# Performance work log

Hardware: AMD Instinct MI355X
Metric: run time of the kernel (lower is better)

## Reference

```python
import jax, jax.numpy as jnp
import numpy as np

B, C, IN, H = 64, 128, 1024, 512  # batch, channels, input features (=='seq_length' arg), hidden


def setup_inputs() -> dict:
    key = jax.random.key(0)
    ks = jax.random.split(key, 9)
    s = 1.0 / np.sqrt(H)  # PyTorch LSTM init: U(-1/sqrt(H), 1/sqrt(H))
    u = lambda k, shape: jax.random.uniform(k, shape, jnp.float32, -s, s)
    return {
        "x": jax.random.normal(ks[0], (B, C, IN), jnp.float32),
        # layer 0: one weight set per direction (fwd, bwd)
        "W_ih0": u(ks[1], (2, 4 * H, IN)),
        "W_hh0": u(ks[2], (2, 4 * H, H)),
        "b_ih0": u(ks[3], (2, 4 * H)),
        "b_hh0": u(ks[4], (2, 4 * H)),
        # layers 1..2: input is concat of both directions (2H)
        "W_ih12": u(ks[5], (2, 2, 4 * H, 2 * H)),
        "W_hh12": u(ks[6], (2, 2, 4 * H, H)),
        "b_ih12": u(ks[7], (2, 2, 4 * H)),
        "b_hh12": u(ks[8], (2, 2, 4 * H)),
    }


def _cell(inp, W_ih, b_ih, b_hh):
    # One LSTM step from zero state (h0 = c0 = 0): W_hh @ h0 == 0, f*c0 == 0.
    gates = inp @ W_ih.T + b_ih + b_hh  # [N, 4H]
    i, f, g, o = jnp.split(gates, 4, axis=-1)  # PyTorch gate order: i, f, g, o
    c = jax.nn.sigmoid(i) * jnp.tanh(g)
    return jax.nn.sigmoid(o) * jnp.tanh(c)  # h, shape [N, H]


def reference(x, W_ih0, W_hh0, b_ih0, b_hh0, W_ih12, W_hh12, b_ih12, b_hh12):
    b, c, n = x.shape
    # Each channel is an independent seq-len-1 LSTM call with zero init state,
    # so fold channels into the batch dimension. W_hh* contribute nothing (h0=0).
    xb = x.reshape(b * c, n)
    h = jnp.concatenate(
        [_cell(xb, W_ih0[d], b_ih0[d], b_hh0[d]) for d in range(2)], axis=-1
    )  # [b*c, 2H]
    for l in range(2):  # layers 1 and 2
        h = jnp.concatenate(
            [_cell(h, W_ih12[l, d], b_ih12[l, d], b_hh12[l, d]) for d in range(2)],
            axis=-1,
        )
    return h.reshape(b, c, 2 * H)  # [batch, channels, 2*hidden]
```

## Files before the change

### kernel.cpp

```cpp
#include <hip/hip_runtime.h>


typedef float f32x4 __attribute__((ext_vector_type(4)));
typedef short short8 __attribute__((ext_vector_type(8)));
typedef unsigned short u16;

#define NP 3072
#define MROWS 8192
#define KDIM 1024
#define BM 256
#define BN 192
#define BK 32
#define LDS_TILE 28672

__device__ __forceinline__ u16 f2bf(float f) {
  unsigned u = __float_as_uint(f);
  u += 0x7fffu + ((u >> 16) & 1u);
  return (u16)(u >> 16);
}
__device__ __forceinline__ float sigmoid_f(float x) {
  return 1.0f / (1.0f + __expf(-x));
}
__device__ __forceinline__ float tanh_f(float x) {
  float xc = fminf(fmaxf(x, -15.0f), 15.0f);
  float e = __expf(2.0f * xc);
  return (e - 1.0f) / (e + 1.0f);
}
__device__ __forceinline__ void gload_lds16(const void* g, void* l) {
  __builtin_amdgcn_global_load_lds((const __attribute__((address_space(1))) void*)g,
                                   (__attribute__((address_space(3))) void*)l,
                                   16, 0, 0);
}


__global__ __launch_bounds__(256) void k_convert_x(const float* __restrict__ x,
                                                   u16* __restrict__ out) {
  int tid = blockIdx.x * 256 + threadIdx.x;
  const float4* src = (const float4*)x + (size_t)tid * 2;
  float4 v0 = src[0], v1 = src[1];
  union { u16 u[8]; uint4 v; } r;
  r.u[0] = f2bf(v0.x); r.u[1] = f2bf(v0.y); r.u[2] = f2bf(v0.z); r.u[3] = f2bf(v0.w);
  r.u[4] = f2bf(v1.x); r.u[5] = f2bf(v1.y); r.u[6] = f2bf(v1.z); r.u[7] = f2bf(v1.w);
  ((uint4*)out)[tid] = r.v;
}

__global__ __launch_bounds__(256) void k_pack_w(const float* __restrict__ Wih0,
                                                const float* __restrict__ Wih12,
                                                u16* __restrict__ P) {
  int tid = blockIdx.x * 256 + threadIdx.x;
  int s   = tid / (NP * 128);
  int rem = tid - s * (NP * 128);
  int p   = rem >> 7;
  int k8  = rem & 127;
  int hb = p / 48;
  int pr = p - hb * 48;
  int gs = pr >> 4;
  int hl = pr & 15;
  int hcol = hb * 16 + hl;
  int dir = hcol >> 9;
  int h   = hcol & 511;
  int og  = (gs == 0) ? 0 : (gs + 1);
  const float* src;
  if (s == 0)
    src = Wih0 + ((size_t)(dir * 2048 + og * 512 + h)) * 1024 + k8 * 8;
  else
    src = Wih12 + ((size_t)(((s - 1) * 2 + dir) * 2048 + og * 512 + h)) * 1024 + k8 * 8;
  float4 v0 = ((const float4*)src)[0];
  float4 v1 = ((const float4*)src)[1];
  union { u16 u[8]; uint4 v; } r;
  r.u[0] = f2bf(v0.x); r.u[1] = f2bf(v0.y); r.u[2] = f2bf(v0.z); r.u[3] = f2bf(v0.w);
  r.u[4] = f2bf(v1.x); r.u[5] = f2bf(v1.y); r.u[6] = f2bf(v1.z); r.u[7] = f2bf(v1.w);
  ((uint4*)P)[tid] = r.v;
}

__global__ __launch_bounds__(256) void k_pack_bias(const float* __restrict__ bih0,
                                                   const float* __restrict__ bhh0,
                                                   const float* __restrict__ bih12,
                                                   const float* __restrict__ bhh12,
                                                   float* __restrict__ pb) {
  int tid = blockIdx.x * 256 + threadIdx.x;
  if (tid >= 3 * NP) return;
  int s = tid / NP;
  int p = tid - s * NP;
  int hb = p / 48;
  int pr = p - hb * 48;
  int gs = pr >> 4;
  int hl = pr & 15;
  int hcol = hb * 16 + hl;
  int dir = hcol >> 9;
  int h   = hcol & 511;
  int og  = (gs == 0) ? 0 : (gs + 1);
  int j   = og * 512 + h;
  float v;
  if (s == 0) {
    int i = dir * 2048 + j;
    v = bih0[i] + bhh0[i];
  } else {
    int i = ((s - 1) * 2 + dir) * 2048 + j;
    v = bih12[i] + bhh12[i];
  }
  pb[tid] = v;
}


#define BAR()    __builtin_amdgcn_s_barrier()
#define SCHEDB() __builtin_amdgcn_sched_barrier(0)
#define WAITV(N) asm volatile("s_waitcnt vmcnt(" #N ")" ::: "memory")
#define MM(Macc, Aop, Bop) Macc = __builtin_amdgcn_mfma_f32_16x16x32_bf16(Aop, Bop, Macc, 0, 0, 0)

#define STAGE(BUF, KT) \
  { char* dst = lds + (BUF) * LDS_TILE + t * 16; \
    gload_lds16(srcA + (size_t)(KT) * BK,               dst); \
    gload_lds16(srcA + 64 * KDIM + (size_t)(KT) * BK,   dst + 4096); \
    gload_lds16(srcA + 128 * KDIM + (size_t)(KT) * BK,  dst + 8192); \
    gload_lds16(srcA + 192 * KDIM + (size_t)(KT) * BK,  dst + 12288); \
    gload_lds16(srcB + (size_t)(KT) * BK,               dst + 16384); \
    gload_lds16(srcB + 64 * KDIM + (size_t)(KT) * BK,   dst + 20480); \
    gload_lds16(srcB + 128 * KDIM + (size_t)(KT) * BK,  dst + 24576); }

#define KSTEP(RBUF, KT, DOST, LASTT) \
  { \
    if (DOST) { STAGE((RBUF)^1, (KT)+1); } \
    const char* base = lds + (RBUF) * LDS_TILE; \
    short8 a0 = *(const short8*)(base + aBase); \
    short8 a1 = *(const short8*)(base + aBase + 1024); \
    short8 a2 = *(const short8*)(base + aBase + 2048); \
    short8 a3 = *(const short8*)(base + aBase + 3072); \
    short8 b0 = *(const short8*)(base + bBase); \
    short8 b1 = *(const short8*)(base + bBase + 1024); \
    short8 b2 = *(const short8*)(base + bBase + 2048); \
    short8 b3 = *(const short8*)(base + bBase + 3072); \
    short8 b4 = *(const short8*)(base + bBase + 4096); \
    short8 b5 = *(const short8*)(base + bBase + 5120); \
    __builtin_amdgcn_s_setprio(1); \
    MM(acc[0][0], a0, b0); MM(acc[1][0], a1, b0); MM(acc[2][0], a2, b0); MM(acc[3][0], a3, b0); \
    MM(acc[0][1], a0, b1); MM(acc[1][1], a1, b1); MM(acc[2][1], a2, b1); MM(acc[3][1], a3, b1); \
    MM(acc[0][2], a0, b2); MM(acc[1][2], a1, b2); MM(acc[2][2], a2, b2); MM(acc[3][2], a3, b2); \
    MM(acc[0][3], a0, b3); MM(acc[1][3], a1, b3); MM(acc[2][3], a2, b3); MM(acc[3][3], a3, b3); \
    MM(acc[0][4], a0, b4); MM(acc[1][4], a1, b4); MM(acc[2][4], a2, b4); MM(acc[3][4], a3, b4); \
    MM(acc[0][5], a0, b5); MM(acc[1][5], a1, b5); MM(acc[2][5], a2, b5); MM(acc[3][5], a3, b5); \
    __builtin_amdgcn_s_setprio(0); \
    a0 = *(const short8*)(base + aBase + 4096); \
    a1 = *(const short8*)(base + aBase + 5120); \
    a2 = *(const short8*)(base + aBase + 6144); \
    a3 = *(const short8*)(base + aBase + 7168); \
    __builtin_amdgcn_s_setprio(1); \
    MM(acc[4][0], a0, b0); MM(acc[5][0], a1, b0); MM(acc[6][0], a2, b0); MM(acc[7][0], a3, b0); \
    MM(acc[4][1], a0, b1); MM(acc[5][1], a1, b1); MM(acc[6][1], a2, b1); MM(acc[7][1], a3, b1); \
    MM(acc[4][2], a0, b2); MM(acc[5][2], a1, b2); MM(acc[6][2], a2, b2); MM(acc[7][2], a3, b2); \
    MM(acc[4][3], a0, b3); MM(acc[5][3], a1, b3); MM(acc[6][3], a2, b3); MM(acc[7][3], a3, b3); \
    MM(acc[4][4], a0, b4); MM(acc[5][4], a1, b4); MM(acc[6][4], a2, b4); MM(acc[7][4], a3, b4); \
    MM(acc[4][5], a0, b5); MM(acc[5][5], a1, b5); MM(acc[6][5], a2, b5); MM(acc[7][5], a3, b5); \
    __builtin_amdgcn_s_setprio(0); \
    if (!(LASTT)) { WAITV(0); BAR(); SCHEDB(); } \
  }

template <bool F32OUT>
__global__ __launch_bounds__(256) void k_lstm_gemm2b(const u16* __restrict__ A,
                                                     const u16* __restrict__ Bp,
                                                     const float* __restrict__ bias,
                                                     void* __restrict__ outp) {
  __shared__ __align__(16) char lds[2 * LDS_TILE];
  const int t    = threadIdx.x;
  const int lane = t & 63;
  const int w    = t >> 6;
  const int wr   = w >> 1;
  const int wc   = w & 1;
  const int r16  = lane & 15, kg = lane >> 4;

  const int n_hw = blockIdx.y * gridDim.x + blockIdx.x;
  const int c    = n_hw & 7;
  const int wlc  = n_hw >> 3;
  const int bx   = (c & 1) * 8 + (wlc & 7);
  const int by   = (c >> 1) * 8 + (wlc >> 3);
  const int brow = by * BM;
  const int bn0  = bx * BN;

  const int slot = (kg ^ ((r16 >> 1) & 3)) << 4;
  const int aBase = wr * 8192 + r16 * 64 + slot;
  const int bBase = 16384 + wc * 6144 + r16 * 64 + slot;

  const int srow = t >> 2;
  const int koct = ((t & 3) ^ ((t >> 3) & 3)) << 3;
  const u16* srcA = A  + (size_t)(brow + srow) * KDIM + koct;
  const u16* srcB = Bp + (size_t)(bn0  + srow) * KDIM + koct;

  f32x4 acc[8][6];
#pragma unroll
  for (int m = 0; m < 8; ++m)
#pragma unroll
    for (int n = 0; n < 6; ++n) acc[m][n] = (f32x4){0.f, 0.f, 0.f, 0.f};

  STAGE(0, 0);
  WAITV(0);
  BAR(); SCHEDB();

  for (int k2 = 0; k2 < 15; ++k2) {
    KSTEP(0, 2 * k2, 1, 0);
    KSTEP(1, 2 * k2 + 1, 1, 0);
  }
  KSTEP(0, 30, 1, 0);
  KSTEP(1, 31, 0, 1);

#pragma unroll
  for (int trio = 0; trio < 2; ++trio) {
    int pbase = bn0 + wc * 96 + trio * 48;
    float biV = bias[pbase + r16];
    float bgV = bias[pbase + 16 + r16];
    float boV = bias[pbase + 32 + r16];
    int hcol = (bx * 4 + wc * 2 + trio) * 16 + r16;
#pragma unroll
    for (int m = 0; m < 8; ++m) {
      int rowb = brow + wr * 128 + m * 16 + kg * 4;
#pragma unroll
      for (int r = 0; r < 4; ++r) {
        float vi = acc[m][trio * 3 + 0][r] + biV;
        float vg = acc[m][trio * 3 + 1][r] + bgV;
        float vo = acc[m][trio * 3 + 2][r] + boV;
        float c2 = sigmoid_f(vi) * tanh_f(vg);
        float hv = sigmoid_f(vo) * tanh_f(c2);
        size_t oidx = (size_t)(rowb + r) * 1024 + hcol;
        if (F32OUT) ((float*)outp)[oidx] = hv;
        else        ((u16*)outp)[oidx]   = f2bf(hv);
      }
    }
  }
}

extern "C" void kernel_launch(void* const* d_in, const int* in_sizes, int n_in,
                              void* d_out, int out_size, void* d_ws, size_t ws_size,
                              hipStream_t stream) {
  const float* x     = (const float*)d_in[0];
  const float* Wih0  = (const float*)d_in[1];
  const float* bih0  = (const float*)d_in[3];
  const float* bhh0  = (const float*)d_in[4];
  const float* Wih12 = (const float*)d_in[5];
  const float* bih12 = (const float*)d_in[7];
  const float* bhh12 = (const float*)d_in[8];

  char* ws = (char*)d_ws;
  u16*   xbf = (u16*)ws;
  u16*   h1  = (u16*)(ws + 16777216);
  u16*   h2  = (u16*)(ws + 33554432);
  u16*   P3  = (u16*)(ws + 50331648);
  float* pb3 = (float*)(ws + 69206016);

  k_convert_x<<<4096, 256, 0, stream>>>(x, xbf);
  k_pack_w<<<4608, 256, 0, stream>>>(Wih0, Wih12, P3);
  k_pack_bias<<<36, 256, 0, stream>>>(bih0, bhh0, bih12, bhh12, pb3);

  dim3 grid(NP / BN, MROWS / BM);
  k_lstm_gemm2b<false><<<grid, 256, 0, stream>>>(xbf, P3, pb3, h1);
  k_lstm_gemm2b<false><<<grid, 256, 0, stream>>>(h1, P3 + (size_t)NP * KDIM, pb3 + NP, h2);
  k_lstm_gemm2b<true ><<<grid, 256, 0, stream>>>(h2, P3 + (size_t)2 * NP * KDIM, pb3 + 2 * NP, d_out);
}
```

Before: 228.4 us.

## Switch GEMM to 512-thread blocks with triple-buffered LDS pipeline

```diff
diff --git a/kernel.cpp b/kernel.cpp
--- a/kernel.cpp
+++ b/kernel.cpp
@@ -110,17 +110,14 @@
 
 #define STAGE(BUF, KT) \
   { char* dst = lds + (BUF) * LDS_TILE + t * 16; \
-    gload_lds16(srcA + (size_t)(KT) * BK,               dst); \
-    gload_lds16(srcA + 64 * KDIM + (size_t)(KT) * BK,   dst + 4096); \
-    gload_lds16(srcA + 128 * KDIM + (size_t)(KT) * BK,  dst + 8192); \
-    gload_lds16(srcA + 192 * KDIM + (size_t)(KT) * BK,  dst + 12288); \
-    gload_lds16(srcB + (size_t)(KT) * BK,               dst + 16384); \
-    gload_lds16(srcB + 64 * KDIM + (size_t)(KT) * BK,   dst + 20480); \
-    gload_lds16(srcB + 128 * KDIM + (size_t)(KT) * BK,  dst + 24576); }
-
-#define KSTEP(RBUF, KT, DOST, LASTT) \
+    gload_lds16(srcA + (size_t)(KT) * BK,              dst); \
+    gload_lds16(srcA + 128 * KDIM + (size_t)(KT) * BK, dst + 8192); \
+    gload_lds16(srcB + (size_t)(KT) * BK,              dst + 16384); \
+    if (t < 256) { gload_lds16(srcB + 128 * KDIM + (size_t)(KT) * BK, dst + 24576); } }
+
+#define KSTEP(RBUF, SBUF, KT, DOST, LASTT) \
   { \
-    if (DOST) { STAGE((RBUF)^1, (KT)+1); } \
+    if (DOST) { STAGE(SBUF, (KT) + 2); } \
     const char* base = lds + (RBUF) * LDS_TILE; \
     short8 a0 = *(const short8*)(base + aBase); \
     short8 a1 = *(const short8*)(base + aBase + 1024); \
@@ -140,27 +137,17 @@
     MM(acc[0][4], a0, b4); MM(acc[1][4], a1, b4); MM(acc[2][4], a2, b4); MM(acc[3][4], a3, b4); \
     MM(acc[0][5], a0, b5); MM(acc[1][5], a1, b5); MM(acc[2][5], a2, b5); MM(acc[3][5], a3, b5); \
     __builtin_amdgcn_s_setprio(0); \
-    a0 = *(const short8*)(base + aBase + 4096); \
-    a1 = *(const short8*)(base + aBase + 5120); \
-    a2 = *(const short8*)(base + aBase + 6144); \
-    a3 = *(const short8*)(base + aBase + 7168); \
-    __builtin_amdgcn_s_setprio(1); \
-    MM(acc[4][0], a0, b0); MM(acc[5][0], a1, b0); MM(acc[6][0], a2, b0); MM(acc[7][0], a3, b0); \
-    MM(acc[4][1], a0, b1); MM(acc[5][1], a1, b1); MM(acc[6][1], a2, b1); MM(acc[7][1], a3, b1); \
-    MM(acc[4][2], a0, b2); MM(acc[5][2], a1, b2); MM(acc[6][2], a2, b2); MM(acc[7][2], a3, b2); \
-    MM(acc[4][3], a0, b3); MM(acc[5][3], a1, b3); MM(acc[6][3], a2, b3); MM(acc[7][3], a3, b3); \
-    MM(acc[4][4], a0, b4); MM(acc[5][4], a1, b4); MM(acc[6][4], a2, b4); MM(acc[7][4], a3, b4); \
-    MM(acc[4][5], a0, b5); MM(acc[5][5], a1, b5); MM(acc[6][5], a2, b5); MM(acc[7][5], a3, b5); \
-    __builtin_amdgcn_s_setprio(0); \
-    if (!(LASTT)) { WAITV(0); BAR(); SCHEDB(); } \
+    if (DOST) { if (t < 256) { WAITV(4); } else { WAITV(3); } } \
+    else if (!(LASTT)) { WAITV(0); } \
+    if (!(LASTT)) { BAR(); SCHEDB(); } \
   }
 
 template <bool F32OUT>
-__global__ __launch_bounds__(256) void k_lstm_gemm2b(const u16* __restrict__ A,
-                                                     const u16* __restrict__ Bp,
-                                                     const float* __restrict__ bias,
-                                                     void* __restrict__ outp) {
-  __shared__ __align__(16) char lds[2 * LDS_TILE];
+__global__ __launch_bounds__(512) void k_lstm_tri(const u16* __restrict__ A,
+                                                  const u16* __restrict__ Bp,
+                                                  const float* __restrict__ bias,
+                                                  void* __restrict__ outp) {
+  __shared__ __align__(16) char lds[3 * LDS_TILE];
   const int t    = threadIdx.x;
   const int lane = t & 63;
   const int w    = t >> 6;
@@ -177,7 +164,7 @@
   const int bn0  = bx * BN;
 
   const int slot = (kg ^ ((r16 >> 1) & 3)) << 4;
-  const int aBase = wr * 8192 + r16 * 64 + slot;
+  const int aBase = wr * 4096 + r16 * 64 + slot;
   const int bBase = 16384 + wc * 6144 + r16 * 64 + slot;
 
   const int srow = t >> 2;
@@ -185,22 +172,24 @@
   const u16* srcA = A  + (size_t)(brow + srow) * KDIM + koct;
   const u16* srcB = Bp + (size_t)(bn0  + srow) * KDIM + koct;
 
-  f32x4 acc[8][6];
-#pragma unroll
-  for (int m = 0; m < 8; ++m)
+  f32x4 acc[4][6];
+#pragma unroll
+  for (int m = 0; m < 4; ++m)
 #pragma unroll
     for (int n = 0; n < 6; ++n) acc[m][n] = (f32x4){0.f, 0.f, 0.f, 0.f};
 
   STAGE(0, 0);
-  WAITV(0);
+  STAGE(1, 1);
+  if (t < 256) { WAITV(4); } else { WAITV(3); }
   BAR(); SCHEDB();
 
-  for (int k2 = 0; k2 < 15; ++k2) {
-    KSTEP(0, 2 * k2, 1, 0);
-    KSTEP(1, 2 * k2 + 1, 1, 0);
-  }
-  KSTEP(0, 30, 1, 0);
-  KSTEP(1, 31, 0, 1);
+  for (int k3 = 0; k3 < 10; ++k3) {
+    KSTEP(0, 2, k3 * 3 + 0, 1, 0);
+    KSTEP(1, 0, k3 * 3 + 1, 1, 0);
+    KSTEP(2, 1, k3 * 3 + 2, 1, 0);
+  }
+  KSTEP(0, 0, 30, 0, 0);
+  KSTEP(1, 0, 31, 0, 1);
 
 #pragma unroll
   for (int trio = 0; trio < 2; ++trio) {
@@ -210,8 +199,8 @@
     float boV = bias[pbase + 32 + r16];
     int hcol = (bx * 4 + wc * 2 + trio) * 16 + r16;
 #pragma unroll
-    for (int m = 0; m < 8; ++m) {
-      int rowb = brow + wr * 128 + m * 16 + kg * 4;
+    for (int m = 0; m < 4; ++m) {
+      int rowb = brow + wr * 64 + m * 16 + kg * 4;
 #pragma unroll
       for (int r = 0; r < 4; ++r) {
         float vi = acc[m][trio * 3 + 0][r] + biV;
@@ -250,7 +239,7 @@
   k_pack_bias<<<36, 256, 0, stream>>>(bih0, bhh0, bih12, bhh12, pb3);
 
   dim3 grid(NP / BN, MROWS / BM);
-  k_lstm_gemm2b<false><<<grid, 256, 0, stream>>>(xbf, P3, pb3, h1);
-  k_lstm_gemm2b<false><<<grid, 256, 0, stream>>>(h1, P3 + (size_t)NP * KDIM, pb3 + NP, h2);
-  k_lstm_gemm2b<true ><<<grid, 256, 0, stream>>>(h2, P3 + (size_t)2 * NP * KDIM, pb3 + 2 * NP, d_out);
-}
+  k_lstm_tri<false><<<grid, 512, 0, stream>>>(xbf, P3, pb3, h1);
+  k_lstm_tri<false><<<grid, 512, 0, stream>>>(h1, P3 + (size_t)NP * KDIM, pb3 + NP, h2);
+  k_lstm_tri<true ><<<grid, 512, 0, stream>>>(h2, P3 + (size_t)2 * NP * KDIM, pb3 + 2 * NP, d_out);
+}
```

Result: faster. 207.0 us (-9.4%).
